# Optimization experiments

Hardware: AMD Instinct MI355X
Metric: run time of the kernel (lower is better)

Reference implementation:

```python
import jax, jax.numpy as jnp
import numpy as np
import math

B, S, E, H, DK, DV = 2, 2048, 1024, 16, 64, 64
EPS = 1e-06


def setup_inputs() -> dict:
    key = jax.random.key(0)
    ks = jax.random.split(key, 11)
    s_in = 1.0 / math.sqrt(E)
    return {
        "query": jax.random.normal(ks[0], (B, S, E), jnp.float32),
        "key_in": jax.random.normal(ks[1], (B, S, E), jnp.float32),
        "value_in": jax.random.normal(ks[2], (B, S, E), jnp.float32),
        "residual_x": jax.random.normal(ks[3], (B, S, E), jnp.float32),
        # stacked per-head Linear params (torch Linear: y = x @ W.T + b); here W stored as [H, E, d]
        "Wq": jax.random.uniform(ks[4], (H, E, DK), jnp.float32, -s_in, s_in),
        "bq": jax.random.uniform(ks[5], (H, DK), jnp.float32, -s_in, s_in),
        "Wk": jax.random.uniform(ks[6], (H, E, DK), jnp.float32, -s_in, s_in),
        "bk": jax.random.uniform(ks[7], (H, DK), jnp.float32, -s_in, s_in),
        "Wv": jax.random.uniform(ks[8], (H, E, DV), jnp.float32, -s_in, s_in),
        "bv": jax.random.uniform(ks[9], (H, DV), jnp.float32, -s_in, s_in),
        "ln_scale": jnp.ones((E,), jnp.float32),
        "ln_shift": jnp.zeros((E,), jnp.float32),
    }


def reference(query, key_in, value_in, residual_x, Wq, bq, Wk, bk, Wv, bv, ln_scale, ln_shift):
    # batched per-head projections (replaces python loop over heads)
    q = jnp.einsum("bse,hed->bhsd", query, Wq) + bq[None, :, None, :]
    k = jnp.einsum("bse,hed->bhsd", key_in, Wk) + bk[None, :, None, :]
    v = jnp.einsum("bse,hed->bhsd", value_in, Wv) + bv[None, :, None, :]
    scores = jnp.einsum("bhsd,bhtd->bhst", q, k) / math.sqrt(DK)  # [B,H,S,S]
    causal = jnp.tril(jnp.ones((S, S), bool))  # mask strictly-upper triangle to -inf
    scores = jnp.where(causal[None, None], scores, -jnp.inf)
    attn = jax.nn.softmax(scores, axis=-1)
    out = jnp.einsum("bhst,bhtd->bhsd", attn, v)
    # concat heads along feature dim (head order = cat order)
    out = out.transpose(0, 2, 1, 3).reshape(B, S, H * DV)
    x = out + residual_x
    # custom LayerNorm: unbiased std, shift added into denominator
    mean = x.mean(-1, keepdims=True)
    std = jnp.sqrt(jnp.sum((x - mean) ** 2, axis=-1, keepdims=True) / (E - 1))
    div = std + EPS + ln_shift  # broadcasts [B,S,1]+[E] -> [B,S,E]
    return ln_scale * (x - mean) / div
```

## Files before the change

kernel.cpp:

```cpp
#include <hip/hip_runtime.h>
#include <hip/hip_bf16.h>

#define NB 2
#define NS 2048
#define NE 1024
#define NH 16
#define ND 64
#define MTOT (NB * NS)

#define QSCALE 0.18033688011112042f

typedef __attribute__((ext_vector_type(8))) short bf8_t;
typedef __attribute__((ext_vector_type(4))) short bf4_t;
typedef __attribute__((ext_vector_type(4))) float f32x4;
typedef __attribute__((ext_vector_type(16))) float f32x16;

__device__ __forceinline__ short f2bf(float f) {
    union { float f; unsigned u; } v; v.f = f;
    return (short)((v.u + 0x7FFFu + ((v.u >> 16) & 1u)) >> 16);
}

__device__ __forceinline__ unsigned cvtpk(float lo, float hi) {
    unsigned r;
    asm("v_cvt_pk_bf16_f32 %0, %1, %2" : "=v"(r) : "v"(lo), "v"(hi));
    return r;
}

__device__ __forceinline__ bf8_t mk4(unsigned a, unsigned b, unsigned c, unsigned d) {
    union { unsigned u[4]; bf8_t v; } t;
    t.u[0] = a; t.u[1] = b; t.u[2] = c; t.u[3] = d;
    return t.v;
}

#define GLOAD16(g, l) __builtin_amdgcn_global_load_lds( \
    (const __attribute__((address_space(1))) void*)(g), \
    (__attribute__((address_space(3))) void*)(l), 16, 0, 0)

__global__ __launch_bounds__(256) void conv_kernel(
    const float* __restrict__ src, short* __restrict__ out)
{
    const size_t nchunk = (size_t)MTOT * NE / 8;
    const size_t stride = (size_t)gridDim.x * 256;
    for (size_t i = (size_t)blockIdx.x * 256 + threadIdx.x; i < nchunk; i += stride) {
        size_t e = i * 8;
        float4 x0 = *(const float4*)(src + e);
        float4 x1 = *(const float4*)(src + e + 4);
        bf8_t o;
        o[0] = f2bf(x0.x); o[1] = f2bf(x0.y); o[2] = f2bf(x0.z); o[3] = f2bf(x0.w);
        o[4] = f2bf(x1.x); o[5] = f2bf(x1.y); o[6] = f2bf(x1.z); o[7] = f2bf(x1.w);
        *(bf8_t*)(out + e) = o;
    }
}

__global__ __launch_bounds__(256) void wt_kernel(
    const float* __restrict__ Wq, const float* __restrict__ Wk, const float* __restrict__ Wv,
    short* __restrict__ wt)
{
    const int p = blockIdx.x / NH, h = blockIdx.x % NH;
    const int e0 = blockIdx.y * 64;
    const float* W = (p == 0) ? Wq : (p == 1) ? Wk : Wv;
    const int t = threadIdx.x;
    const int er = t >> 2, dc = (t & 3) * 16;
    const float* src = W + ((size_t)h * NE + e0 + er) * ND + dc;
    short* dst = wt + (size_t)(p * NH + h) * ND * NE;
#pragma unroll
    for (int j = 0; j < 16; j += 4) {
        float4 x = *(const float4*)(src + j);
        dst[(size_t)(dc + j + 0) * NE + e0 + er] = f2bf(x.x);
        dst[(size_t)(dc + j + 1) * NE + e0 + er] = f2bf(x.y);
        dst[(size_t)(dc + j + 2) * NE + e0 + er] = f2bf(x.z);
        dst[(size_t)(dc + j + 3) * NE + e0 + er] = f2bf(x.w);
    }
}

__global__ __launch_bounds__(256) void proj_kernel(
    const short* __restrict__ in_bf, const short* __restrict__ wt,
    const float* __restrict__ bq, const float* __restrict__ bk, const float* __restrict__ bv,
    short* __restrict__ q_ws, short* __restrict__ k_ws, short* __restrict__ vT_ws,
    int pbase)
{
    __shared__ __attribute__((aligned(16))) short As[128 * 32];
    __shared__ __attribute__((aligned(16))) short Bs[128 * 32];

    const int z = blockIdx.z, p = pbase + z;
    const short* A = in_bf + (size_t)z * MTOT * NE;
    const short* Bm = wt + (size_t)p * NE * NE;
    const float* bias_all = (p == 0) ? bq : (p == 1) ? bk : bv;
    const float oscale = (p == 0) ? QSCALE : 1.0f;

    const int m0 = blockIdx.x * 128, n0 = blockIdx.y * 128;
    const int t = threadIdx.x, lane = t & 63, w = t >> 6;
    const int l15 = lane & 15, g = lane >> 4;
    const int wr = w >> 1, wc = w & 1;

    const int srow = t >> 2, scol = (t & 3) * 8;
    const short* ag = A + (size_t)(m0 + srow) * NE + scol;
    const short* bg = Bm + (size_t)(n0 + srow) * NE + scol;
    short* asl = As + t * 8;
    short* bsl = Bs + t * 8;

    f32x4 acc[4][4];
#pragma unroll
    for (int i = 0; i < 4; ++i)
#pragma unroll
        for (int j = 0; j < 4; ++j) acc[i][j] = (f32x4){0.f, 0.f, 0.f, 0.f};

    for (int k0 = 0; k0 < NE; k0 += 32) {
        __syncthreads();
        GLOAD16(ag + k0, asl);
        GLOAD16(ag + k0 + (size_t)64 * NE, asl + 2048);
        GLOAD16(bg + k0, bsl);
        GLOAD16(bg + k0 + (size_t)64 * NE, bsl + 2048);
        __syncthreads();
        bf8_t af[4], bfr[4];
#pragma unroll
        for (int mf = 0; mf < 4; ++mf)
            af[mf] = *(const bf8_t*)&As[(wr * 64 + mf * 16 + l15) * 32 + g * 8];
#pragma unroll
        for (int nf = 0; nf < 4; ++nf)
            bfr[nf] = *(const bf8_t*)&Bs[(wc * 64 + nf * 16 + l15) * 32 + g * 8];
#pragma unroll
        for (int mf = 0; mf < 4; ++mf)
#pragma unroll
            for (int nf = 0; nf < 4; ++nf)
                acc[mf][nf] = __builtin_amdgcn_mfma_f32_16x16x32_bf16(af[mf], bfr[nf], acc[mf][nf], 0, 0, 0);
    }

    const int h = (n0 + wc * 64) >> 6;
    const float* bias = bias_all + h * ND;

    if (p < 2) {
        short* outp = (p == 0) ? q_ws : k_ws;
#pragma unroll
        for (int mf = 0; mf < 4; ++mf) {
            const int m = m0 + wr * 64 + mf * 16 + g * 4;
            const int bb = m >> 11, s = m & (NS - 1);
#pragma unroll
            for (int nf = 0; nf < 4; ++nf) {
                const int d = nf * 16 + l15;
                const float bi = bias[d];
                short* op = outp + (((size_t)bb * NH + h) * NS + s) * ND + d;
#pragma unroll
                for (int r = 0; r < 4; ++r)
                    op[(size_t)r * ND] = f2bf((acc[mf][nf][r] + bi) * oscale);
            }
        }
    } else {
#pragma unroll
        for (int mf = 0; mf < 4; ++mf) {
            const int m = m0 + wr * 64 + mf * 16 + g * 4;
            const int bb = m >> 11, s = m & (NS - 1);
#pragma unroll
            for (int nf = 0; nf < 4; ++nf) {
                const int d = nf * 16 + l15;
                const float bi = bias[d];
                bf4_t pk;
#pragma unroll
                for (int r = 0; r < 4; ++r) pk[r] = f2bf(acc[mf][nf][r] + bi);
                *(bf4_t*)&vT_ws[(((size_t)bb * NH + h) * ND + d) * NS + s] = pk;
            }
        }
    }
}

__global__ __launch_bounds__(256, 2) void attn_kernel(
    const short* __restrict__ q_ws, const short* __restrict__ k_ws,
    const short* __restrict__ vT_ws, float* __restrict__ O)
{
    __shared__ float oT[4][32][65];
    const int t = threadIdx.x, lane = t & 63, w = t >> 6;
    const int g = (int)blockIdx.x * 4 + w;
    const int jq = 63 - (g >> 5);
    const int bh = g & 31;
    const int b = bh >> 4, h = bh & 15;
    const int q0w = jq * 32;
    const int nt = (jq >> 1) + 1;
    const int l31 = lane & 31, hi = lane >> 5;
    const size_t base = (size_t)bh * NS * ND;

    bf8_t Qf[4];
    {
        const short* qsrc = q_ws + base + (size_t)(q0w + l31) * ND + hi * 8;
#pragma unroll
        for (int s = 0; s < 4; ++s) Qf[s] = *(const bf8_t*)(qsrc + s * 16);
    }

    f32x16 Oa[2];
#pragma unroll
    for (int rb = 0; rb < 2; ++rb)
#pragma unroll
        for (int r = 0; r < 16; ++r) Oa[rb][r] = 0.f;
    float m_i = -1e30f, l_i = 0.f;
    const int qg = q0w + l31;

    for (int tt = 0; tt < nt; ++tt) {
        const int t0 = tt * 64;

        bf8_t Kf[2][4];
#pragma unroll
        for (int c = 0; c < 2; ++c) {
            const short* kp = k_ws + base + (size_t)(t0 + c * 32 + l31) * ND + hi * 8;
#pragma unroll
            for (int s = 0; s < 4; ++s) Kf[c][s] = *(const bf8_t*)(kp + s * 16);
        }
        bf8_t Vf[4][2];
#pragma unroll
        for (int rb = 0; rb < 2; ++rb) {
            const short* vp = vT_ws + base + (size_t)(rb * 32 + l31) * NS + t0 + hi * 8;
#pragma unroll
            for (int cs = 0; cs < 4; ++cs) Vf[cs][rb] = *(const bf8_t*)(vp + cs * 16);
        }

        f32x16 Sv[2];
#pragma unroll
        for (int c = 0; c < 2; ++c) {
#pragma unroll
            for (int r = 0; r < 16; ++r) Sv[c][r] = 0.f;
#pragma unroll
            for (int s = 0; s < 4; ++s)
                Sv[c] = __builtin_amdgcn_mfma_f32_32x32x16_bf16(Kf[c][s], Qf[s], Sv[c], 0, 0, 0);
        }

        if (tt == nt - 1) {
#pragma unroll
            for (int c = 0; c < 2; ++c)
#pragma unroll
                for (int r = 0; r < 16; ++r) {
                    const int kvg = t0 + c * 32 + (r & 3) + 8 * (r >> 2) + 4 * hi;
                    if (kvg > qg) Sv[c][r] = -1e30f;
                }
        }

        float mloc = Sv[0][0];
#pragma unroll
        for (int r = 1; r < 16; ++r) mloc = fmaxf(mloc, Sv[0][r]);
#pragma unroll
        for (int r = 0; r < 16; ++r) mloc = fmaxf(mloc, Sv[1][r]);
        mloc = fmaxf(mloc, __shfl_xor(mloc, 32));

        if (__any(mloc > m_i + 11.0f)) {
            const float mn = fmaxf(m_i, mloc);
            const float al = exp2f(m_i - mn);
            m_i = mn;
            l_i *= al;
#pragma unroll
            for (int rb = 0; rb < 2; ++rb)
#pragma unroll
                for (int r = 0; r < 16; ++r) Oa[rb][r] *= al;
        }

        float rs = 0.f;
        bf8_t Pf[2][2];
#pragma unroll
        for (int c = 0; c < 2; ++c) {
#pragma unroll
            for (int r = 0; r < 16; ++r) {
                const float pv = exp2f(Sv[c][r] - m_i);
                Sv[c][r] = pv;
                rs += pv;
            }
            unsigned wv[8], xv[8];
#pragma unroll
            for (int i = 0; i < 8; ++i) wv[i] = cvtpk(Sv[c][2 * i], Sv[c][2 * i + 1]);
#pragma unroll
            for (int i = 0; i < 8; ++i) xv[i] = __shfl_xor(wv[i], 32);
            Pf[c][0] = hi ? mk4(xv[2], xv[3], wv[2], wv[3]) : mk4(wv[0], wv[1], xv[0], xv[1]);
            Pf[c][1] = hi ? mk4(xv[6], xv[7], wv[6], wv[7]) : mk4(wv[4], wv[5], xv[4], xv[5]);
        }
        rs += __shfl_xor(rs, 32);
        l_i += rs;

#pragma unroll
        for (int cs = 0; cs < 4; ++cs)
#pragma unroll
            for (int rb = 0; rb < 2; ++rb)
                Oa[rb] = __builtin_amdgcn_mfma_f32_32x32x16_bf16(Vf[cs][rb], Pf[cs >> 1][cs & 1], Oa[rb], 0, 0, 0);
    }

    const float inv = 1.0f / l_i;
#pragma unroll
    for (int rb = 0; rb < 2; ++rb)
#pragma unroll
        for (int r = 0; r < 16; ++r)
            oT[w][l31][rb * 32 + (r & 3) + 8 * (r >> 2) + 4 * hi] = Oa[rb][r] * inv;

    asm volatile("s_waitcnt lgkmcnt(0)" ::: "memory");

#pragma unroll
    for (int p4 = 0; p4 < 4; ++p4) {
        const int qr = p4 * 8 + (lane >> 3), d8 = (lane & 7) * 8;
        const float4 a0 = *(const float4*)&oT[w][qr][d8];
        const float4 a1 = *(const float4*)&oT[w][qr][d8 + 4];
        float* op = O + ((size_t)b * NS + q0w + qr) * NE + h * 64 + d8;
        *(float4*)op = a0;
        *(float4*)(op + 4) = a1;
    }
}

__global__ __launch_bounds__(256) void ln_kernel(
    const float* __restrict__ Oin, const float* __restrict__ resid,
    const float* __restrict__ ln_scale, const float* __restrict__ ln_shift,
    float* __restrict__ out)
{
    __shared__ float red[8];
    const int row = blockIdx.x, t = threadIdx.x;
    const size_t basei = (size_t)row * NE + t * 4;
    float4 x = *(const float4*)(Oin + basei);
    float4 rr = *(const float4*)(resid + basei);
    x.x += rr.x; x.y += rr.y; x.z += rr.z; x.w += rr.w;
    float ps = x.x + x.y + x.z + x.w;
#pragma unroll
    for (int off = 32; off; off >>= 1) ps += __shfl_xor(ps, off);
    if ((t & 63) == 0) red[t >> 6] = ps;
    __syncthreads();
    const float mean = (red[0] + red[1] + red[2] + red[3]) * (1.0f / NE);
    const float dx0 = x.x - mean, dx1 = x.y - mean, dx2 = x.z - mean, dx3 = x.w - mean;
    float ss = dx0 * dx0 + dx1 * dx1 + dx2 * dx2 + dx3 * dx3;
#pragma unroll
    for (int off = 32; off; off >>= 1) ss += __shfl_xor(ss, off);
    if ((t & 63) == 0) red[4 + (t >> 6)] = ss;
    __syncthreads();
    const float stdv = sqrtf((red[4] + red[5] + red[6] + red[7]) * (1.0f / (NE - 1)));
    float4 sc = *(const float4*)(ln_scale + t * 4);
    float4 sh = *(const float4*)(ln_shift + t * 4);
    float4 o;
    o.x = sc.x * dx0 / (stdv + 1e-6f + sh.x);
    o.y = sc.y * dx1 / (stdv + 1e-6f + sh.y);
    o.z = sc.z * dx2 / (stdv + 1e-6f + sh.z);
    o.w = sc.w * dx3 / (stdv + 1e-6f + sh.w);
    *(float4*)(out + basei) = o;
}

extern "C" void kernel_launch(void* const* d_in, const int* in_sizes, int n_in,
                              void* d_out, int out_size, void* d_ws, size_t ws_size,
                              hipStream_t stream) {
    (void)in_sizes; (void)n_in; (void)out_size; (void)ws_size;
    const float* query    = (const float*)d_in[0];
    const float* key_in   = (const float*)d_in[1];
    const float* value_in = (const float*)d_in[2];
    const float* resid    = (const float*)d_in[3];
    const float* Wq = (const float*)d_in[4];
    const float* bq = (const float*)d_in[5];
    const float* Wk = (const float*)d_in[6];
    const float* bk = (const float*)d_in[7];
    const float* Wv = (const float*)d_in[8];
    const float* bv = (const float*)d_in[9];
    const float* ln_scale = (const float*)d_in[10];
    const float* ln_shift = (const float*)d_in[11];
    float* out = (float*)d_out;

    char* ws = (char*)d_ws;
    short* wt_ws = (short*)ws;
    short* in_bf = (short*)(ws + (6u << 20));
    short* q_ws  = (short*)(ws + (22u << 20));
    short* k_ws  = (short*)(ws + (30u << 20));
    short* vT_ws = (short*)(ws + (38u << 20));
    float* O_ws  = (float*)ws;

    short* slot0 = in_bf;
    short* slot1 = in_bf + (size_t)MTOT * NE;

    wt_kernel<<<dim3(3 * NH, NE / 64), 256, 0, stream>>>(Wq, Wk, Wv, wt_ws);

    conv_kernel<<<1024, 256, 0, stream>>>(query, slot0);
    conv_kernel<<<1024, 256, 0, stream>>>(key_in, slot1);
    proj_kernel<<<dim3(MTOT / 128, NE / 128, 2), 256, 0, stream>>>(
        in_bf, wt_ws, bq, bk, bv, q_ws, k_ws, vT_ws, 0);

    conv_kernel<<<1024, 256, 0, stream>>>(value_in, slot0);
    proj_kernel<<<dim3(MTOT / 128, NE / 128, 1), 256, 0, stream>>>(
        in_bf, wt_ws, bq, bk, bv, q_ws, k_ws, vT_ws, 2);

    attn_kernel<<<512, 256, 0, stream>>>(q_ws, k_ws, vT_ws, O_ws);
    ln_kernel<<<dim3(NB * NS), 256, 0, stream>>>(O_ws, resid, ln_scale, ln_shift, out);
}
```

Measured before the change: 285.0 us.

## Fuse prep kernels, single 3-way projection launch, LDS double-buffered attention

Merges the weight transpose and the three input conversions into one prep kernel. The weight transpose now goes through LDS so writes are coalesced, and rounding uses the packed convert instruction. The three projections run as one launch. The attention kernel now has each block of four waves share one head and stage K/V tiles into swizzled, double-buffered LDS with async global-to-LDS loads, using XCD-aware block mapping. This cuts redundant per-wave global K/V reads and overlaps loads with compute. The costs are per-tile barriers, idle waves on the causal tail within a block, and a larger workspace footprint.

```diff
diff --git a/kernel.cpp b/kernel.cpp
--- a/kernel.cpp
+++ b/kernel.cpp
@@ -19,13 +19,11 @@
     union { float f; unsigned u; } v; v.f = f;
     return (short)((v.u + 0x7FFFu + ((v.u >> 16) & 1u)) >> 16);
 }
-
 __device__ __forceinline__ unsigned cvtpk(float lo, float hi) {
     unsigned r;
     asm("v_cvt_pk_bf16_f32 %0, %1, %2" : "=v"(r) : "v"(lo), "v"(hi));
     return r;
 }
-
 __device__ __forceinline__ bf8_t mk4(unsigned a, unsigned b, unsigned c, unsigned d) {
     union { unsigned u[4]; bf8_t v; } t;
     t.u[0] = a; t.u[1] = b; t.u[2] = c; t.u[3] = d;
@@ -36,61 +34,69 @@
     (const __attribute__((address_space(1))) void*)(g), \
     (__attribute__((address_space(3))) void*)(l), 16, 0, 0)
 
-__global__ __launch_bounds__(256) void conv_kernel(
-    const float* __restrict__ src, short* __restrict__ out)
+__global__ __launch_bounds__(256) void prep_kernel(
+    const float* __restrict__ query, const float* __restrict__ key_in, const float* __restrict__ value_in,
+    const float* __restrict__ Wq, const float* __restrict__ Wk, const float* __restrict__ Wv,
+    short* __restrict__ wt, short* __restrict__ in_bf)
 {
-    const size_t nchunk = (size_t)MTOT * NE / 8;
-    const size_t stride = (size_t)gridDim.x * 256;
-    for (size_t i = (size_t)blockIdx.x * 256 + threadIdx.x; i < nchunk; i += stride) {
-        size_t e = i * 8;
-        float4 x0 = *(const float4*)(src + e);
-        float4 x1 = *(const float4*)(src + e + 4);
-        bf8_t o;
-        o[0] = f2bf(x0.x); o[1] = f2bf(x0.y); o[2] = f2bf(x0.z); o[3] = f2bf(x0.w);
-        o[4] = f2bf(x1.x); o[5] = f2bf(x1.y); o[6] = f2bf(x1.z); o[7] = f2bf(x1.w);
-        *(bf8_t*)(out + e) = o;
-    }
-}
-
-__global__ __launch_bounds__(256) void wt_kernel(
-    const float* __restrict__ Wq, const float* __restrict__ Wk, const float* __restrict__ Wv,
-    short* __restrict__ wt)
-{
-    const int p = blockIdx.x / NH, h = blockIdx.x % NH;
-    const int e0 = blockIdx.y * 64;
-    const float* W = (p == 0) ? Wq : (p == 1) ? Wk : Wv;
-    const int t = threadIdx.x;
-    const int er = t >> 2, dc = (t & 3) * 16;
-    const float* src = W + ((size_t)h * NE + e0 + er) * ND + dc;
-    short* dst = wt + (size_t)(p * NH + h) * ND * NE;
-#pragma unroll
-    for (int j = 0; j < 16; j += 4) {
-        float4 x = *(const float4*)(src + j);
-        dst[(size_t)(dc + j + 0) * NE + e0 + er] = f2bf(x.x);
-        dst[(size_t)(dc + j + 1) * NE + e0 + er] = f2bf(x.y);
-        dst[(size_t)(dc + j + 2) * NE + e0 + er] = f2bf(x.z);
-        dst[(size_t)(dc + j + 3) * NE + e0 + er] = f2bf(x.w);
+    __shared__ float T[64][68];
+    const int bid = (int)blockIdx.x, t = threadIdx.x;
+    if (bid < 768) {
+        const int hb = bid >> 4;
+        const int p = hb >> 4, h = hb & 15;
+        const int e0 = (bid & 15) << 6;
+        const float* W = (p == 0) ? Wq : (p == 1) ? Wk : Wv;
+        const int er = t >> 2, dc = (t & 3) * 16;
+        const float* src = W + ((size_t)h * NE + e0 + er) * ND + dc;
+#pragma unroll
+        for (int j = 0; j < 16; j += 4) {
+            float4 x = *(const float4*)(src + j);
+            T[er][dc + j + 0] = x.x; T[er][dc + j + 1] = x.y;
+            T[er][dc + j + 2] = x.z; T[er][dc + j + 3] = x.w;
+        }
+        __syncthreads();
+        const int dr = t >> 2, ec = (t & 3) * 16;
+        float v[16];
+#pragma unroll
+        for (int j = 0; j < 16; ++j) v[j] = T[ec + j][dr];
+        short* dst = wt + (size_t)p * NE * NE + (size_t)(h * 64 + dr) * NE + e0 + ec;
+        *(bf8_t*)dst = mk4(cvtpk(v[0], v[1]), cvtpk(v[2], v[3]),
+                           cvtpk(v[4], v[5]), cvtpk(v[6], v[7]));
+        *(bf8_t*)(dst + 8) = mk4(cvtpk(v[8], v[9]), cvtpk(v[10], v[11]),
+                                 cvtpk(v[12], v[13]), cvtpk(v[14], v[15]));
+    } else {
+        const size_t nchunk = (size_t)3 * MTOT * NE / 8;
+        const size_t stride = (size_t)1280 * 256;
+        for (size_t i = (size_t)(bid - 768) * 256 + t; i < nchunk; i += stride) {
+            size_t e = i * 8;
+            int p = (int)(e >> 22);
+            const float* src = (p == 0) ? query : (p == 1) ? key_in : value_in;
+            size_t off = e & ((1ull << 22) - 1);
+            float4 x0 = *(const float4*)(src + off);
+            float4 x1 = *(const float4*)(src + off + 4);
+            *(bf8_t*)(in_bf + e) = mk4(cvtpk(x0.x, x0.y), cvtpk(x0.z, x0.w),
+                                       cvtpk(x1.x, x1.y), cvtpk(x1.z, x1.w));
+        }
     }
 }
 
 __global__ __launch_bounds__(256) void proj_kernel(
     const short* __restrict__ in_bf, const short* __restrict__ wt,
     const float* __restrict__ bq, const float* __restrict__ bk, const float* __restrict__ bv,
-    short* __restrict__ q_ws, short* __restrict__ k_ws, short* __restrict__ vT_ws,
-    int pbase)
+    short* __restrict__ q_ws, short* __restrict__ k_ws, short* __restrict__ vT_ws)
 {
     __shared__ __attribute__((aligned(16))) short As[128 * 32];
     __shared__ __attribute__((aligned(16))) short Bs[128 * 32];
 
-    const int z = blockIdx.z, p = pbase + z;
-    const short* A = in_bf + (size_t)z * MTOT * NE;
+    const int p = blockIdx.z;
+    const short* A = in_bf + (size_t)p * MTOT * NE;
     const short* Bm = wt + (size_t)p * NE * NE;
     const float* bias_all = (p == 0) ? bq : (p == 1) ? bk : bv;
     const float oscale = (p == 0) ? QSCALE : 1.0f;
 
     const int m0 = blockIdx.x * 128, n0 = blockIdx.y * 128;
     const int t = threadIdx.x, lane = t & 63, w = t >> 6;
-    const int l15 = lane & 15, g = lane >> 4;
+    const int l15 = lane & 15, g = lane >> 4, g8 = g * 8;
     const int wr = w >> 1, wc = w & 1;
 
     const int srow = t >> 2, scol = (t & 3) * 8;
@@ -115,10 +121,10 @@
         bf8_t af[4], bfr[4];
 #pragma unroll
         for (int mf = 0; mf < 4; ++mf)
-            af[mf] = *(const bf8_t*)&As[(wr * 64 + mf * 16 + l15) * 32 + g * 8];
+            af[mf] = *(const bf8_t*)&As[(wr * 64 + mf * 16 + l15) * 32 + g8];
 #pragma unroll
         for (int nf = 0; nf < 4; ++nf)
-            bfr[nf] = *(const bf8_t*)&Bs[(wc * 64 + nf * 16 + l15) * 32 + g * 8];
+            bfr[nf] = *(const bf8_t*)&Bs[(wc * 64 + nf * 16 + l15) * 32 + g8];
 #pragma unroll
         for (int mf = 0; mf < 4; ++mf)
 #pragma unroll
@@ -163,20 +169,36 @@
     }
 }
 
-__global__ __launch_bounds__(256, 2) void attn_kernel(
+__global__ __launch_bounds__(256) void attn_kernel(
     const short* __restrict__ q_ws, const short* __restrict__ k_ws,
     const short* __restrict__ vT_ws, float* __restrict__ O)
 {
-    __shared__ float oT[4][32][65];
+    __shared__ __attribute__((aligned(16))) short KV[2][2][64 * 64];
+
     const int t = threadIdx.x, lane = t & 63, w = t >> 6;
-    const int g = (int)blockIdx.x * 4 + w;
-    const int jq = 63 - (g >> 5);
-    const int bh = g & 31;
+    const int xcd = (int)blockIdx.x & 7, idx = (int)blockIdx.x >> 3;
+    const int a = 15 - (idx >> 2);
+    const int bh = xcd * 4 + (idx & 3);
     const int b = bh >> 4, h = bh & 15;
+    const int jq = 4 * a + w;
     const int q0w = jq * 32;
-    const int nt = (jq >> 1) + 1;
+    const int ntw = (jq >> 1) + 1;
+    const int maxnt = 2 * a + 2;
     const int l31 = lane & 31, hi = lane >> 5;
     const size_t base = (size_t)bh * NS * ND;
+    const int qg = q0w + l31;
+
+    const int r1 = t >> 3;
+    const int cswz = ((t & 7) * 8) ^ ((r1 & 7) << 3);
+    const short* kgb = k_ws + base + (size_t)r1 * ND + cswz;
+    const short* vgb = vT_ws + base + (size_t)r1 * NS + cswz;
+
+#define STAGE(c, t0) do { \
+    GLOAD16(kgb + (size_t)(t0) * ND, &KV[c][0][t * 8]); \
+    GLOAD16(kgb + (size_t)((t0) + 32) * ND, &KV[c][0][2048 + t * 8]); \
+    GLOAD16(vgb + (t0), &KV[c][1][t * 8]); \
+    GLOAD16(vgb + (size_t)32 * NS + (t0), &KV[c][1][2048 + t * 8]); \
+} while (0)
 
     bf8_t Qf[4];
     {
@@ -191,110 +213,131 @@
 #pragma unroll
         for (int r = 0; r < 16; ++r) Oa[rb][r] = 0.f;
     float m_i = -1e30f, l_i = 0.f;
-    const int qg = q0w + l31;
-
-    for (int tt = 0; tt < nt; ++tt) {
-        const int t0 = tt * 64;
-
-        bf8_t Kf[2][4];
-#pragma unroll
-        for (int c = 0; c < 2; ++c) {
-            const short* kp = k_ws + base + (size_t)(t0 + c * 32 + l31) * ND + hi * 8;
-#pragma unroll
-            for (int s = 0; s < 4; ++s) Kf[c][s] = *(const bf8_t*)(kp + s * 16);
-        }
-        bf8_t Vf[4][2];
-#pragma unroll
-        for (int rb = 0; rb < 2; ++rb) {
-            const short* vp = vT_ws + base + (size_t)(rb * 32 + l31) * NS + t0 + hi * 8;
-#pragma unroll
-            for (int cs = 0; cs < 4; ++cs) Vf[cs][rb] = *(const bf8_t*)(vp + cs * 16);
-        }
-
-        f32x16 Sv[2];
-#pragma unroll
-        for (int c = 0; c < 2; ++c) {
-#pragma unroll
-            for (int r = 0; r < 16; ++r) Sv[c][r] = 0.f;
-#pragma unroll
-            for (int s = 0; s < 4; ++s)
-                Sv[c] = __builtin_amdgcn_mfma_f32_32x32x16_bf16(Kf[c][s], Qf[s], Sv[c], 0, 0, 0);
-        }
-
-        if (tt == nt - 1) {
+    const int sw = (l31 & 7) << 3;
+
+    STAGE(0, 0);
+
+    for (int tt = 0; tt < maxnt; ++tt) {
+        const int cur = tt & 1;
+        if (tt + 1 < maxnt) {
+            STAGE(cur ^ 1, (tt + 1) * 64);
+            asm volatile("s_waitcnt vmcnt(4)" ::: "memory");
+        } else {
+            asm volatile("s_waitcnt vmcnt(0)" ::: "memory");
+        }
+        __builtin_amdgcn_sched_barrier(0);
+        __builtin_amdgcn_s_barrier();
+        __builtin_amdgcn_sched_barrier(0);
+
+        if (tt < ntw) {
+            const int t0 = tt * 64;
+            bf8_t Kf[2][4];
 #pragma unroll
             for (int c = 0; c < 2; ++c)
 #pragma unroll
+                for (int s = 0; s < 4; ++s)
+                    Kf[c][s] = *(const bf8_t*)&KV[cur][0][(c * 32 + l31) * 64 + ((s * 16 + hi * 8) ^ sw)];
+
+            f32x16 Sv[2];
+#pragma unroll
+            for (int c = 0; c < 2; ++c) {
+#pragma unroll
+                for (int r = 0; r < 16; ++r) Sv[c][r] = 0.f;
+#pragma unroll
+                for (int s = 0; s < 4; ++s)
+                    Sv[c] = __builtin_amdgcn_mfma_f32_32x32x16_bf16(Kf[c][s], Qf[s], Sv[c], 0, 0, 0);
+            }
+
+            if (tt == ntw - 1) {
+#pragma unroll
+                for (int c = 0; c < 2; ++c)
+#pragma unroll
+                    for (int r = 0; r < 16; ++r) {
+                        const int kvg = t0 + c * 32 + (r & 3) + 8 * (r >> 2) + 4 * hi;
+                        if (kvg > qg) Sv[c][r] = -1e30f;
+                    }
+            }
+
+            float mloc = Sv[0][0];
+#pragma unroll
+            for (int r = 1; r < 16; ++r) mloc = fmaxf(mloc, Sv[0][r]);
+#pragma unroll
+            for (int r = 0; r < 16; ++r) mloc = fmaxf(mloc, Sv[1][r]);
+            mloc = fmaxf(mloc, __shfl_xor(mloc, 32));
+
+            if (__any(mloc > m_i + 11.0f)) {
+                const float mn = fmaxf(m_i, mloc);
+                const float al = exp2f(m_i - mn);
+                m_i = mn;
+                l_i *= al;
+#pragma unroll
+                for (int rb = 0; rb < 2; ++rb)
+#pragma unroll
+                    for (int r = 0; r < 16; ++r) Oa[rb][r] *= al;
+            }
+
+            float rs = 0.f;
+            bf8_t Pf[2][2];
+#pragma unroll
+            for (int c = 0; c < 2; ++c) {
+#pragma unroll
                 for (int r = 0; r < 16; ++r) {
-                    const int kvg = t0 + c * 32 + (r & 3) + 8 * (r >> 2) + 4 * hi;
-                    if (kvg > qg) Sv[c][r] = -1e30f;
+                    const float pv = exp2f(Sv[c][r] - m_i);
+                    Sv[c][r] = pv;
+                    rs += pv;
                 }
-        }
-
-        float mloc = Sv[0][0];
-#pragma unroll
-        for (int r = 1; r < 16; ++r) mloc = fmaxf(mloc, Sv[0][r]);
-#pragma unroll
-        for (int r = 0; r < 16; ++r) mloc = fmaxf(mloc, Sv[1][r]);
-        mloc = fmaxf(mloc, __shfl_xor(mloc, 32));
-
-        if (__any(mloc > m_i + 11.0f)) {
-            const float mn = fmaxf(m_i, mloc);
-            const float al = exp2f(m_i - mn);
-            m_i = mn;
-            l_i *= al;
-#pragma unroll
-            for (int rb = 0; rb < 2; ++rb)
-#pragma unroll
-                for (int r = 0; r < 16; ++r) Oa[rb][r] *= al;
-        }
-
-        float rs = 0.f;
-        bf8_t Pf[2][2];
-#pragma unroll
-        for (int c = 0; c < 2; ++c) {
-#pragma unroll
-            for (int r = 0; r < 16; ++r) {
-                const float pv = exp2f(Sv[c][r] - m_i);
-                Sv[c][r] = pv;
-                rs += pv;
-            }
-            unsigned wv[8], xv[8];
-#pragma unroll
-            for (int i = 0; i < 8; ++i) wv[i] = cvtpk(Sv[c][2 * i], Sv[c][2 * i + 1]);
-#pragma unroll
-            for (int i = 0; i < 8; ++i) xv[i] = __shfl_xor(wv[i], 32);
-            Pf[c][0] = hi ? mk4(xv[2], xv[3], wv[2], wv[3]) : mk4(wv[0], wv[1], xv[0], xv[1]);
-            Pf[c][1] = hi ? mk4(xv[6], xv[7], wv[6], wv[7]) : mk4(wv[4], wv[5], xv[4], xv[5]);
-        }
-        rs += __shfl_xor(rs, 32);
-        l_i += rs;
-
-#pragma unroll
-        for (int cs = 0; cs < 4; ++cs)
-#pragma unroll
-            for (int rb = 0; rb < 2; ++rb)
-                Oa[rb] = __builtin_amdgcn_mfma_f32_32x32x16_bf16(Vf[cs][rb], Pf[cs >> 1][cs & 1], Oa[rb], 0, 0, 0);
-    }
-
+                unsigned wv[8], xv[8];
+#pragma unroll
+                for (int i = 0; i < 8; ++i) wv[i] = cvtpk(Sv[c][2 * i], Sv[c][2 * i + 1]);
+#pragma unroll
+                for (int i = 0; i < 8; ++i) xv[i] = __shfl_xor(wv[i], 32);
+                Pf[c][0] = hi ? mk4(xv[2], xv[3], wv[2], wv[3]) : mk4(wv[0], wv[1], xv[0], xv[1]);
+                Pf[c][1] = hi ? mk4(xv[6], xv[7], wv[6], wv[7]) : mk4(wv[4], wv[5], xv[4], xv[5]);
+            }
+            rs += __shfl_xor(rs, 32);
+            l_i += rs;
+
+#pragma unroll
+            for (int cs = 0; cs < 4; ++cs) {
+#pragma unroll
+                for (int rb = 0; rb < 2; ++rb) {
+                    const bf8_t vf = *(const bf8_t*)&KV[cur][1][(rb * 32 + l31) * 64 + ((cs * 16 + hi * 8) ^ sw)];
+                    Oa[rb] = __builtin_amdgcn_mfma_f32_32x32x16_bf16(vf, Pf[cs >> 1][cs & 1], Oa[rb], 0, 0, 0);
+                }
+            }
+        }
+        __builtin_amdgcn_sched_barrier(0);
+        __builtin_amdgcn_s_barrier();
+        __builtin_amdgcn_sched_barrier(0);
+    }
+
+    __syncthreads();
+
+    float* oTw = (float*)(&KV[0][0][0]) + w * (32 * 36);
     const float inv = 1.0f / l_i;
 #pragma unroll
-    for (int rb = 0; rb < 2; ++rb)
-#pragma unroll
-        for (int r = 0; r < 16; ++r)
-            oT[w][l31][rb * 32 + (r & 3) + 8 * (r >> 2) + 4 * hi] = Oa[rb][r] * inv;
-
-    asm volatile("s_waitcnt lgkmcnt(0)" ::: "memory");
-
-#pragma unroll
-    for (int p4 = 0; p4 < 4; ++p4) {
-        const int qr = p4 * 8 + (lane >> 3), d8 = (lane & 7) * 8;
-        const float4 a0 = *(const float4*)&oT[w][qr][d8];
-        const float4 a1 = *(const float4*)&oT[w][qr][d8 + 4];
-        float* op = O + ((size_t)b * NS + q0w + qr) * NE + h * 64 + d8;
+    for (int rb = 0; rb < 2; ++rb) {
+#pragma unroll
+        for (int r = 0; r < 16; ++r) {
+            const int crow = (r & 3) + 8 * (r >> 2) + 4 * hi;
+            oTw[l31 * 36 + crow] = Oa[rb][r] * inv;
+        }
+        asm volatile("s_waitcnt lgkmcnt(0)" ::: "memory");
+        __builtin_amdgcn_sched_barrier(0);
+        const float* src = &oTw[l31 * 36 + hi * 16];
+        float4 a0 = *(const float4*)(src);
+        float4 a1 = *(const float4*)(src + 4);
+        float4 a2 = *(const float4*)(src + 8);
+        float4 a3 = *(const float4*)(src + 12);
+        float* op = O + ((size_t)b * NS + q0w + l31) * NE + h * 64 + rb * 32 + hi * 16;
         *(float4*)op = a0;
         *(float4*)(op + 4) = a1;
-    }
+        *(float4*)(op + 8) = a2;
+        *(float4*)(op + 12) = a3;
+        asm volatile("s_waitcnt lgkmcnt(0)" ::: "memory");
+        __builtin_amdgcn_sched_barrier(0);
+    }
+#undef STAGE
 }
 
 __global__ __launch_bounds__(256) void ln_kernel(
@@ -350,27 +393,16 @@
     float* out = (float*)d_out;
 
     char* ws = (char*)d_ws;
-    short* wt_ws = (short*)ws;
-    short* in_bf = (short*)(ws + (6u << 20));
-    short* q_ws  = (short*)(ws + (22u << 20));
-    short* k_ws  = (short*)(ws + (30u << 20));
-    short* vT_ws = (short*)(ws + (38u << 20));
+    short* in_bf = (short*)ws;
+    short* wt_ws = (short*)(ws + (24u << 20));
+    short* q_ws  = (short*)(ws + (30u << 20));
+    short* k_ws  = (short*)(ws + (38u << 20));
+    short* vT_ws = (short*)(ws + (46u << 20));
     float* O_ws  = (float*)ws;
 
-    short* slot0 = in_bf;
-    short* slot1 = in_bf + (size_t)MTOT * NE;
-
-    wt_kernel<<<dim3(3 * NH, NE / 64), 256, 0, stream>>>(Wq, Wk, Wv, wt_ws);
-
-    conv_kernel<<<1024, 256, 0, stream>>>(query, slot0);
-    conv_kernel<<<1024, 256, 0, stream>>>(key_in, slot1);
-    proj_kernel<<<dim3(MTOT / 128, NE / 128, 2), 256, 0, stream>>>(
-        in_bf, wt_ws, bq, bk, bv, q_ws, k_ws, vT_ws, 0);
-
-    conv_kernel<<<1024, 256, 0, stream>>>(value_in, slot0);
-    proj_kernel<<<dim3(MTOT / 128, NE / 128, 1), 256, 0, stream>>>(
-        in_bf, wt_ws, bq, bk, bv, q_ws, k_ws, vT_ws, 2);
-
+    prep_kernel<<<2048, 256, 0, stream>>>(query, key_in, value_in, Wq, Wk, Wv, wt_ws, in_bf);
+    proj_kernel<<<dim3(MTOT / 128, NE / 128, 3), 256, 0, stream>>>(
+        in_bf, wt_ws, bq, bk, bv, q_ws, k_ws, vT_ws);
     attn_kernel<<<512, 256, 0, stream>>>(q_ws, k_ws, vT_ws, O_ws);
     ln_kernel<<<dim3(NB * NS), 256, 0, stream>>>(O_ws, resid, ln_scale, ln_shift, out);
 }
```

Result: faster. 241.9 us (-15.1%).
